# Kernel tuning notes

Measured on AMD Instinct MI355X. Metric: run time of the kernel, lower is better.

The kernel has to match this reference:

```python
import jax, jax.numpy as jnp
import numpy as np

N, E = 2048, 6144
DV_IN, DV_OUT = 128, 64
DE_IN, DE_OUT = 16, 16


def setup_inputs() -> dict:
    key = jax.random.key(0)
    ks = jax.random.split(key, 11)
    return {
        "H_v": jax.random.normal(ks[0], (N, DV_IN), jnp.float32),
        "H_e": jax.random.normal(ks[1], (E, DE_IN), jnp.float32),
        "adj_v": jax.random.uniform(ks[2], (N, N), jnp.float32),
        "adj_e": jax.random.uniform(ks[3], (E, E), jnp.float32),
        "T": jax.random.normal(ks[4], (N, E), jnp.float32),
        "W_v": jax.random.normal(ks[5], (DV_IN, DV_OUT), jnp.float32) * (1.0 / np.sqrt(DV_OUT)),
        "b_v": jax.random.normal(ks[6], (DV_OUT,), jnp.float32) * 0.01,
        "p_v": jax.random.normal(ks[7], (1, DE_IN), jnp.float32),
        "W_e": jax.random.normal(ks[8], (DE_IN, DE_OUT), jnp.float32) * (1.0 / np.sqrt(DE_OUT)),
        "b_e": jax.random.normal(ks[9], (DE_OUT,), jnp.float32) * 0.01,
        "p_e": jax.random.normal(ks[10], (1, DV_OUT), jnp.float32),
    }


def reference(H_v, H_e, adj_v, adj_e, T, W_v, b_v, p_v, W_e, b_e, p_e):
    n, e = T.shape
    # ---- node layer (AlternateConvolution, node_layer=True) ----
    d_e = (H_e @ p_v.T)[:, 0]                      # [E] per-edge diag values
    mult1 = (T * d_e[None, :]) @ T.T               # T @ diag(d_e) @ T^T -> [N,N]
    idx_n = jnp.arange(n)
    M1 = mult1.at[idx_n, idx_n].set(1.0)           # eye*1 + (1-eye)*multiplier
    adjusted_Av = M1 * adj_v
    Hv_out = adjusted_Av @ (H_v @ W_v) + b_v       # [N, DV_OUT]
    # ---- edge layer (AlternateConvolution, node_layer=False) ----
    d_v = (Hv_out @ p_e.T)[:, 0]                   # [N] per-node diag values
    mult2 = (T.T * d_v[None, :]) @ T               # T^T @ diag(d_v) @ T -> [E,E]
    idx_e = jnp.arange(e)
    M2 = mult2.at[idx_e, idx_e].set(1.0)
    adjusted_Ae = M2 * adj_e
    norm_Ae = adjusted_Ae / (adjusted_Ae.max(axis=0, keepdims=True) + 1e-10)
    He_out = norm_Ae @ (H_e @ W_e) + b_e           # [E, DE_OUT]
    return Hv_out, He_out
```

## Files before the change

### kernel.cpp

```cpp
#include <hip/hip_runtime.h>

typedef unsigned short u16;
typedef unsigned int u32;
typedef __bf16 bf16x8 __attribute__((ext_vector_type(8)));
typedef float f32x4 __attribute__((ext_vector_type(4)));

#define NN 2048
#define NE 6144
#define DVIN 128
#define DVOUT 64
#define DEIN 16
#define DEOUT 16

#define BM 128
#define BN 128
#define BK 64
#define MS 132

__device__ __forceinline__ u16 f2b(float f) {
  __bf16 b = (__bf16)f;
  return __builtin_bit_cast(u16, b);
}

__device__ __forceinline__ float b2f(u16 u) {
  return __uint_as_float(((u32)u) << 16);
}

__device__ __forceinline__ void async16(const void* g, void* l) {
  __builtin_amdgcn_global_load_lds(
      (const __attribute__((address_space(1))) void*)g,
      (__attribute__((address_space(3))) void*)l, 16, 0, 0);
}

__device__ __forceinline__ bf16x8 load8(const u16* p) {
  union { uint4 u; bf16x8 b; } w;
  w.u = *(const uint4*)p;
  return w.b;
}


__global__ __launch_bounds__(256) void k_de(const float* __restrict__ He,
                                            const float* __restrict__ pv,
                                            float* __restrict__ de) {
  int j = blockIdx.x * 256 + threadIdx.x;
  float s = 0.f;
#pragma unroll
  for (int k = 0; k < DEIN; k++) s += He[j * DEIN + k] * pv[k];
  de[j] = s;
}

__global__ __launch_bounds__(256) void k_tb(const float* __restrict__ T,
                                            const float* __restrict__ de,
                                            u16* __restrict__ Tb,
                                            u16* __restrict__ Tbs) {
  size_t idx = (size_t)blockIdx.x * 256 + threadIdx.x;
  size_t f = idx * 8;
  float4 v0 = *(const float4*)(T + f);
  float4 v1 = *(const float4*)(T + f + 4);
  int col = (int)(f % (size_t)NE);
  float4 d0 = *(const float4*)(de + col);
  float4 d1 = *(const float4*)(de + col + 4);
  float v[8] = {v0.x, v0.y, v0.z, v0.w, v1.x, v1.y, v1.z, v1.w};
  float d[8] = {d0.x, d0.y, d0.z, d0.w, d1.x, d1.y, d1.z, d1.w};
  union { u16 s[8]; uint4 u; } a, b;
#pragma unroll
  for (int j = 0; j < 8; j++) { a.s[j] = f2b(v[j]); b.s[j] = f2b(v[j] * d[j]); }
  *(uint4*)(Tb + f) = a.u;
  *(uint4*)(Tbs + f) = b.u;
}

__global__ __launch_bounds__(256) void k_x(const float* __restrict__ Hv,
                                           const float* __restrict__ Wv,
                                           u16* __restrict__ Xt) {
  int i = blockIdx.x * 256 + threadIdx.x;
  int d = blockIdx.y;
  float s = 0.f;
#pragma unroll 8
  for (int k = 0; k < DVIN; k++) s += Hv[i * DVIN + k] * Wv[k * DVOUT + d];
  Xt[(size_t)d * NN + i] = f2b(s);
}

__global__ __launch_bounds__(256) void k_dv(const float* __restrict__ HvOut,
                                            const float* __restrict__ pe,
                                            float* __restrict__ dv) {
  int i = blockIdx.x * 256 + threadIdx.x;
  float s = 0.f;
#pragma unroll
  for (int c = 0; c < DVOUT; c++) s += HvOut[i * DVOUT + c] * pe[c];
  dv[i] = s;
}

__global__ __launch_bounds__(256) void k_tt(const float* __restrict__ T,
                                            const float* __restrict__ dv,
                                            u16* __restrict__ Tt,
                                            u16* __restrict__ Tts) {
  __shared__ float tile[32][33];
  int tx = threadIdx.x, ty = threadIdx.y;
  int bx = blockIdx.x, by = blockIdx.y;
  int col = bx * 32 + tx;
#pragma unroll
  for (int r = 0; r < 4; r++) {
    int row = by * 32 + ty + r * 8;
    tile[ty + r * 8][tx] = T[(size_t)row * NE + col];
  }
  __syncthreads();
  int ocol = by * 32 + tx;
  float dvv = dv[ocol];
#pragma unroll
  for (int r = 0; r < 4; r++) {
    int orow = bx * 32 + ty + r * 8;
    float v = tile[tx][ty + r * 8];
    Tt[(size_t)orow * NN + ocol] = f2b(v);
    Tts[(size_t)orow * NN + ocol] = f2b(v * dvv);
  }
}

__global__ __launch_bounds__(256) void k_zt(const float* __restrict__ He,
                                            const float* __restrict__ We,
                                            const u32* __restrict__ colmax,
                                            u16* __restrict__ Ztb) {
  int b = blockIdx.x * 256 + threadIdx.x;
  float h[16];
  const float4* hp = (const float4*)(He + (size_t)b * DEIN);
#pragma unroll
  for (int q = 0; q < 4; q++) {
    float4 t = hp[q];
    h[q * 4 + 0] = t.x; h[q * 4 + 1] = t.y; h[q * 4 + 2] = t.z; h[q * 4 + 3] = t.w;
  }
  float inv = 1.0f / (__uint_as_float(colmax[b]) + 1e-10f);
#pragma unroll
  for (int d = 0; d < DEOUT; d++) {
    float s = 0.f;
#pragma unroll
    for (int k = 0; k < DEIN; k++) s += h[k] * We[k * DEOUT + d];
    Ztb[(size_t)d * NE + b] = f2b(s * inv);
  }
}

__device__ __forceinline__ void tile_loop(const u16* __restrict__ A,
                                          const u16* __restrict__ B,
                                          int bm0, int bn0, int K,
                                          int kbeg, int kend,
                                          u16* As, u16* Bs,
                                          f32x4 (&acc)[4][4]) {
  const int t = threadIdx.x;
  const int lane = t & 63;
  const int lr = lane & 15, kg = lane >> 4;
  const int wave = t >> 6;
  const int wm = (wave >> 1) * 64, wn = (wave & 1) * 64;

  const int arow = t >> 3;
  const int acolsw = (((t & 7) ^ (arow & 7)) * 8);
  const u16* Ag = A + (size_t)(bm0 + arow) * K + acolsw;
  const u16* Bg = B + (size_t)(bn0 + arow) * K + acolsw;
  u16* Al = &As[t * 8];
  u16* Bl = &Bs[t * 8];

  for (int k0 = kbeg; k0 < kend; k0 += BK) {
    __syncthreads();
#pragma unroll
    for (int r = 0; r < 4; r++) {
      async16(Ag + (size_t)(r * 32) * K + k0, Al + r * 32 * BK);
      async16(Bg + (size_t)(r * 32) * K + k0, Bl + r * 32 * BK);
    }
    __syncthreads();
#pragma unroll
    for (int kk = 0; kk < BK; kk += 32) {
      bf16x8 af[4], bf[4];
#pragma unroll
      for (int mi = 0; mi < 4; mi++) {
        int row = wm + mi * 16 + lr;
        int c = (kk >> 3) + kg;
        af[mi] = load8(&As[row * BK + ((c ^ (row & 7)) << 3)]);
      }
#pragma unroll
      for (int ni = 0; ni < 4; ni++) {
        int row = wn + ni * 16 + lr;
        int c = (kk >> 3) + kg;
        bf[ni] = load8(&Bs[row * BK + ((c ^ (row & 7)) << 3)]);
      }
#pragma unroll
      for (int mi = 0; mi < 4; mi++)
#pragma unroll
        for (int ni = 0; ni < 4; ni++)
          acc[mi][ni] = __builtin_amdgcn_mfma_f32_16x16x32_bf16(
              af[mi], bf[ni], acc[mi][ni], 0, 0, 0);
    }
  }
}

__global__ __launch_bounds__(256) void gemm_sym1(const u16* __restrict__ A,
                                                 const u16* __restrict__ B,
                                                 float* __restrict__ P) {
  const int bi = blockIdx.y, bj = blockIdx.x;
  if (bj < bi) return;
  __shared__ u16 As[BM * BK];
  __shared__ u16 Bs[BN * BK];
  const int bm0 = bi * BM, bn0 = bj * BN;
  const int K = NE, kc = NE / 4;
  f32x4 acc[4][4];
#pragma unroll
  for (int i = 0; i < 4; i++)
#pragma unroll
    for (int j = 0; j < 4; j++) acc[i][j] = (f32x4){0.f, 0.f, 0.f, 0.f};

  tile_loop(A, B, bm0, bn0, K, blockIdx.z * kc, (blockIdx.z + 1) * kc, As, Bs, acc);

  const int t = threadIdx.x, lane = t & 63, lr = lane & 15, kg = lane >> 4;
  const int wave = t >> 6, wm = (wave >> 1) * 64, wn = (wave & 1) * 64;
  float* Pz = P + (size_t)blockIdx.z * NN * NN;
#pragma unroll
  for (int ni = 0; ni < 4; ni++) {
    const int cj = bn0 + wn + ni * 16 + lr;
#pragma unroll
    for (int mi = 0; mi < 4; mi++)
#pragma unroll
      for (int r = 0; r < 4; r++) {
        const int ci = bm0 + wm + mi * 16 + kg * 4 + r;
        Pz[(size_t)ci * NN + cj] = acc[mi][ni][r];
      }
  }
}

__global__ __launch_bounds__(256) void k_comb(const float* __restrict__ P,
                                              const float* __restrict__ adj,
                                              u16* __restrict__ A1) {
  const int bi = blockIdx.y, bj = blockIdx.x;
  if (bj < bi) return;
  __shared__ float tile[128][129];
  const int bm0 = bi * 128, bn0 = bj * 128;
  const int t = threadIdx.x;
  const bool diagb = (bi == bj);
  const size_t NP = (size_t)NN * NN;
  for (int e = t; e < 128 * 32; e += 256) {
    int row = e >> 5, c4 = (e & 31) * 4;
    size_t off = (size_t)(bm0 + row) * NN + bn0 + c4;
    float4 s0 = *(const float4*)(P + off);
    float4 s1 = *(const float4*)(P + NP + off);
    float4 s2 = *(const float4*)(P + 2 * NP + off);
    float4 s3 = *(const float4*)(P + 3 * NP + off);
    float sv[4] = {s0.x + s1.x + s2.x + s3.x, s0.y + s1.y + s2.y + s3.y,
                   s0.z + s1.z + s2.z + s3.z, s0.w + s1.w + s2.w + s3.w};
    if (diagb) {
#pragma unroll
      for (int q = 0; q < 4; q++)
        if (c4 + q == row) sv[q] = 1.0f;
    }
    float4 av = *(const float4*)(adj + off);
    float avv[4] = {av.x, av.y, av.z, av.w};
    union { u16 h[4]; uint2 u; } o;
#pragma unroll
    for (int q = 0; q < 4; q++) {
      tile[row][c4 + q] = sv[q];
      o.h[q] = f2b(sv[q] * avv[q]);
    }
    *(uint2*)(A1 + off) = o.u;
  }
  if (!diagb) {
    __syncthreads();
    for (int e = t; e < 128 * 32; e += 256) {
      int row = e >> 5, c4 = (e & 31) * 4;
      size_t off = (size_t)(bn0 + row) * NN + bm0 + c4;
      float4 av = *(const float4*)(adj + off);
      float avv[4] = {av.x, av.y, av.z, av.w};
      union { u16 h[4]; uint2 u; } o;
#pragma unroll
      for (int q = 0; q < 4; q++) o.h[q] = f2b(tile[c4 + q][row] * avv[q]);
      *(uint2*)(A1 + off) = o.u;
    }
  }
}

__global__ __launch_bounds__(256) void gemm_sym2(const u16* __restrict__ A,
                                                 const u16* __restrict__ B,
                                                 const float* __restrict__ adj,
                                                 u16* __restrict__ C,
                                                 u32* __restrict__ colmax) {
  const int bi = blockIdx.y, bj = blockIdx.x;
  if (bj < bi) return;
  __shared__ union {
    struct { u16 As[BM * BK]; u16 Bs[BN * BK]; } s;
    u16 mir[128 * MS];
  } sh;
  __shared__ u32 cmaxN[128];
  __shared__ u32 cmaxM[128];
  const int bm0 = bi * BM, bn0 = bj * BN;
  const int t = threadIdx.x;
  const int N = NE, K = NN;
  const bool diagb = (bi == bj);
  if (t < 128) { cmaxN[t] = 0u; cmaxM[t] = 0u; }

  f32x4 acc[4][4];
#pragma unroll
  for (int i = 0; i < 4; i++)
#pragma unroll
    for (int j = 0; j < 4; j++) acc[i][j] = (f32x4){0.f, 0.f, 0.f, 0.f};

  tile_loop(A, B, bm0, bn0, K, 0, K, sh.s.As, sh.s.Bs, acc);

  const int lane = t & 63, lr = lane & 15, kg = lane >> 4;
  const int wave = t >> 6, wm = (wave >> 1) * 64, wn = (wave & 1) * 64;

  __syncthreads();

#pragma unroll
  for (int ni = 0; ni < 4; ni++) {
    const int cjl = wn + ni * 16 + lr;
    const int cj = bn0 + cjl;
    float cm = 0.f;
#pragma unroll
    for (int mi = 0; mi < 4; mi++) {
#pragma unroll
      for (int r = 0; r < 4; r++) {
        const int cil = wm + mi * 16 + kg * 4 + r;
        const int ci = bm0 + cil;
        float v = acc[mi][ni][r];
        if (ci == cj) v = 1.0f;
        float w = v * adj[(size_t)ci * N + cj];
        C[(size_t)ci * N + cj] = f2b(w);
        cm = fmaxf(cm, w);
        if (!diagb) sh.mir[cjl * MS + cil] = f2b(v);
      }
    }
    atomicMax(&cmaxN[cjl], __float_as_uint(cm));
  }

  if (!diagb) {
    __syncthreads();
    const int rb = t >> 4, cb = (t & 15) * 8;
    float rmax[8];
#pragma unroll
    for (int q = 0; q < 8; q++) rmax[q] = 0.f;
#pragma unroll
    for (int rr = 0; rr < 8; rr++) {
      const int row = rb + rr * 16;
      union { uint2 u; u16 s[4]; } w0, w1;
      w0.u = *(const uint2*)&sh.mir[row * MS + cb];
      w1.u = *(const uint2*)&sh.mir[row * MS + cb + 4];
      float f[8] = {b2f(w0.s[0]), b2f(w0.s[1]), b2f(w0.s[2]), b2f(w0.s[3]),
                    b2f(w1.s[0]), b2f(w1.s[1]), b2f(w1.s[2]), b2f(w1.s[3])};
      const float* ap = adj + (size_t)(bn0 + row) * N + bm0 + cb;
      float4 a0 = *(const float4*)ap;
      float4 a1 = *(const float4*)(ap + 4);
      float a[8] = {a0.x, a0.y, a0.z, a0.w, a1.x, a1.y, a1.z, a1.w};
      union { u16 s[8]; uint4 u; } o;
#pragma unroll
      for (int q = 0; q < 8; q++) {
        float w = f[q] * a[q];
        rmax[q] = fmaxf(rmax[q], w);
        o.s[q] = f2b(w);
      }
      *(uint4*)&C[(size_t)(bn0 + row) * N + bm0 + cb] = o.u;
    }
#pragma unroll
    for (int q = 0; q < 8; q++)
      atomicMax(&cmaxM[cb + q], __float_as_uint(rmax[q]));
  }

  __syncthreads();
  if (t < 128) {
    atomicMax(&colmax[bn0 + t], cmaxN[t]);
    if (!diagb) atomicMax(&colmax[bm0 + t], cmaxM[t]);
  }
}


__global__ __launch_bounds__(256) void k_hv(const u16* __restrict__ A1,
                                            const u16* __restrict__ Xt,
                                            const float* __restrict__ bv,
                                            float* __restrict__ out) {
  __shared__ float red[4 * 1024];
  const int t = threadIdx.x, wave = t >> 6, lane = t & 63;
  const int lr = lane & 15, kg = lane >> 4;
  const int m0 = blockIdx.x * 16;
  const int K = NN;
  f32x4 acc[4];
#pragma unroll
  for (int i = 0; i < 4; i++) acc[i] = (f32x4){0.f, 0.f, 0.f, 0.f};
  const int kbeg = wave * (K / 4), kend = kbeg + (K / 4);
  for (int k = kbeg; k < kend; k += 32) {
    bf16x8 af = load8(&A1[(size_t)(m0 + lr) * K + k + kg * 8]);
#pragma unroll
    for (int ni = 0; ni < 4; ni++) {
      bf16x8 bfr = load8(&Xt[(size_t)(ni * 16 + lr) * K + k + kg * 8]);
      acc[ni] = __builtin_amdgcn_mfma_f32_16x16x32_bf16(af, bfr, acc[ni], 0, 0, 0);
    }
  }
#pragma unroll
  for (int ni = 0; ni < 4; ni++)
#pragma unroll
    for (int r = 0; r < 4; r++)
      red[wave * 1024 + (kg * 4 + r) * 64 + ni * 16 + lr] = acc[ni][r];
  __syncthreads();
#pragma unroll
  for (int q = 0; q < 4; q++) {
    int e = t + 256 * q;
    int row = e >> 6, col = e & 63;
    float v = red[e] + red[1024 + e] + red[2048 + e] + red[3072 + e] + bv[col];
    out[(size_t)(m0 + row) * DVOUT + col] = v;
  }
}

__global__ __launch_bounds__(256) void k_he(const u16* __restrict__ adjE,
                                            const u16* __restrict__ Ztb,
                                            const float* __restrict__ be,
                                            float* __restrict__ out) {
  __shared__ float red[4 * 256];
  const int t = threadIdx.x, wave = t >> 6, lane = t & 63;
  const int lr = lane & 15, kg = lane >> 4;
  const int m0 = blockIdx.x * 16;
  const int K = NE;
  f32x4 acc = (f32x4){0.f, 0.f, 0.f, 0.f};
  const int kbeg = wave * (K / 4), kend = kbeg + (K / 4);
  for (int k = kbeg; k < kend; k += 32) {
    bf16x8 af = load8(&adjE[(size_t)(m0 + lr) * K + k + kg * 8]);
    bf16x8 bfr = load8(&Ztb[(size_t)lr * K + k + kg * 8]);
    acc = __builtin_amdgcn_mfma_f32_16x16x32_bf16(af, bfr, acc, 0, 0, 0);
  }
#pragma unroll
  for (int r = 0; r < 4; r++)
    red[wave * 256 + (kg * 4 + r) * 16 + lr] = acc[r];
  __syncthreads();
  {
    int row = t >> 4, col = t & 15;
    float v = red[t] + red[256 + t] + red[512 + t] + red[768 + t] + be[col];
    out[(size_t)(m0 + row) * DEOUT + col] = v;
  }
}

extern "C" void kernel_launch(void* const* d_in, const int* in_sizes, int n_in,
                              void* d_out, int out_size, void* d_ws, size_t ws_size,
                              hipStream_t stream) {
  const float* H_v = (const float*)d_in[0];
  const float* H_e = (const float*)d_in[1];
  const float* adj_v = (const float*)d_in[2];
  const float* adj_e = (const float*)d_in[3];
  const float* T = (const float*)d_in[4];
  const float* W_v = (const float*)d_in[5];
  const float* b_v = (const float*)d_in[6];
  const float* p_v = (const float*)d_in[7];
  const float* W_e = (const float*)d_in[8];
  const float* b_e = (const float*)d_in[9];
  const float* p_e = (const float*)d_in[10];
  float* outHv = (float*)d_out;
  float* outHe = (float*)d_out + NN * DVOUT;

  char* ws = (char*)d_ws;
  u16* Tb   = (u16*)(ws + 0);
  u16* Tbs  = (u16*)(ws + 25165824);
  u16* Tt   = (u16*)(ws + 50331648);
  u16* Tts  = (u16*)(ws + 75497472);
  u16* adjE = (u16*)(ws + 100663296);
  u16* A1   = (u16*)(ws + 176160768);
  u16* Xt   = (u16*)(ws + 184549376);
  u16* Ztb  = (u16*)(ws + 184811520);
  float* de = (float*)(ws + 185008128);
  float* dv = (float*)(ws + 185032704);
  u32* cmax = (u32*)(ws + 185040896);
  float* P = (float*)(ws + 50331648);

  k_de<<<NE / 256, 256, 0, stream>>>(H_e, p_v, de);
  k_tb<<<(NN * (size_t)NE) / 8 / 256, 256, 0, stream>>>(T, de, Tb, Tbs);
  k_x<<<dim3(NN / 256, DVOUT), 256, 0, stream>>>(H_v, W_v, Xt);
  gemm_sym1<<<dim3(NN / BN, NN / BM, 4), 256, 0, stream>>>(Tbs, Tb, P);
  k_comb<<<dim3(NN / 128, NN / 128), 256, 0, stream>>>(P, adj_v, A1);
  k_hv<<<NN / 16, 256, 0, stream>>>(A1, Xt, b_v, outHv);
  k_dv<<<NN / 256, 256, 0, stream>>>(outHv, p_e, dv);
  k_tt<<<dim3(NE / 32, NN / 32), dim3(32, 8), 0, stream>>>(T, dv, Tt, Tts);
  hipMemsetAsync(cmax, 0, NE * sizeof(u32), stream);
  gemm_sym2<<<dim3(NE / BN, NE / BM), 256, 0, stream>>>(Tts, Tt, adj_e, adjE, cmax);
  k_zt<<<NE / 256, 256, 0, stream>>>(H_e, W_e, cmax, Ztb);
  k_he<<<NE / 16, 256, 0, stream>>>(adjE, Ztb, b_e, outHe);
}
```

Before: 660.1 us.

## Launch only upper-triangle tiles, pack split-K partials, widen GEMV blocks

The symmetric GEMMs and the combine kernel now launch a 1D grid that covers only upper-triangle tiles, decoded with a sqrt-based triangular index, so lower-triangle blocks no longer launch just to exit. The split-K partials of gemm_sym1 are written as packed per-tile fragments with vector stores, and k_comb unpacks them through shared memory. This replaces strided scalar stores and shrinks the partial buffer. k_hv and k_he switch to 512 threads with 8-way K splits to add memory-level parallelism, at the cost of larger shared reduction buffers.

```diff
diff --git a/kernel.cpp b/kernel.cpp
--- a/kernel.cpp
+++ b/kernel.cpp
@@ -36,6 +36,15 @@
   union { uint4 u; bf16x8 b; } w;
   w.u = *(const uint4*)p;
   return w.b;
+}
+
+__device__ __forceinline__ void tri_decode(int L, int Nt, int& bi, int& bj) {
+  float Nf = (float)Nt + 0.5f;
+  int b = (int)(Nf - sqrtf(Nf * Nf - 2.0f * (float)L));
+  while (b * Nt - (b * (b - 1)) / 2 > L) b--;
+  while ((b + 1) * Nt - ((b + 1) * b) / 2 <= L) b++;
+  bi = b;
+  bj = b + (L - (b * Nt - (b * (b - 1)) / 2));
 }
 
 
@@ -192,72 +201,76 @@
 __global__ __launch_bounds__(256) void gemm_sym1(const u16* __restrict__ A,
                                                  const u16* __restrict__ B,
                                                  float* __restrict__ P) {
-  const int bi = blockIdx.y, bj = blockIdx.x;
-  if (bj < bi) return;
+  const int L = blockIdx.x;
+  const int z = L / 136, tri = L - z * 136;
+  int bi, bj;
+  tri_decode(tri, NN / BM, bi, bj);
   __shared__ u16 As[BM * BK];
   __shared__ u16 Bs[BN * BK];
   const int bm0 = bi * BM, bn0 = bj * BN;
-  const int K = NE, kc = NE / 4;
+  const int kc = NE / 4;
   f32x4 acc[4][4];
 #pragma unroll
   for (int i = 0; i < 4; i++)
 #pragma unroll
     for (int j = 0; j < 4; j++) acc[i][j] = (f32x4){0.f, 0.f, 0.f, 0.f};
 
-  tile_loop(A, B, bm0, bn0, K, blockIdx.z * kc, (blockIdx.z + 1) * kc, As, Bs, acc);
-
-  const int t = threadIdx.x, lane = t & 63, lr = lane & 15, kg = lane >> 4;
-  const int wave = t >> 6, wm = (wave >> 1) * 64, wn = (wave & 1) * 64;
-  float* Pz = P + (size_t)blockIdx.z * NN * NN;
-#pragma unroll
-  for (int ni = 0; ni < 4; ni++) {
-    const int cj = bn0 + wn + ni * 16 + lr;
-#pragma unroll
-    for (int mi = 0; mi < 4; mi++)
-#pragma unroll
-      for (int r = 0; r < 4; r++) {
-        const int ci = bm0 + wm + mi * 16 + kg * 4 + r;
-        Pz[(size_t)ci * NN + cj] = acc[mi][ni][r];
-      }
-  }
+  tile_loop(A, B, bm0, bn0, NE, z * kc, (z + 1) * kc, As, Bs, acc);
+
+  const int t = threadIdx.x;
+  f32x4* P4 = (f32x4*)(P + ((size_t)z * 136 + tri) * (BM * BN) + t * 64);
+#pragma unroll
+  for (int ni = 0; ni < 4; ni++)
+#pragma unroll
+    for (int mi = 0; mi < 4; mi++) P4[ni * 4 + mi] = acc[mi][ni];
 }
 
 __global__ __launch_bounds__(256) void k_comb(const float* __restrict__ P,
                                               const float* __restrict__ adj,
                                               u16* __restrict__ A1) {
-  const int bi = blockIdx.y, bj = blockIdx.x;
-  if (bj < bi) return;
+  const int tri = blockIdx.x;
+  int bi, bj;
+  tri_decode(tri, NN / BM, bi, bj);
   __shared__ float tile[128][129];
   const int bm0 = bi * 128, bn0 = bj * 128;
   const int t = threadIdx.x;
   const bool diagb = (bi == bj);
-  const size_t NP = (size_t)NN * NN;
+  const int lane = t & 63, lr = lane & 15, kg = lane >> 4;
+  const int wave = t >> 6, wm = (wave >> 1) * 64, wn = (wave & 1) * 64;
+
+  const f32x4* P4 = (const f32x4*)(P + (size_t)tri * (BM * BN) + t * 64);
+  const size_t SL = (size_t)136 * BM * BN / 4;
+#pragma unroll
+  for (int ni = 0; ni < 4; ni++) {
+#pragma unroll
+    for (int mi = 0; mi < 4; mi++) {
+      f32x4 s = P4[ni * 4 + mi];
+      f32x4 s1 = P4[SL + ni * 4 + mi];
+      f32x4 s2 = P4[2 * SL + ni * 4 + mi];
+      f32x4 s3 = P4[3 * SL + ni * 4 + mi];
+      s = s + s1 + s2 + s3;
+      const int cil = wm + mi * 16 + kg * 4;
+      const int cjl = wn + ni * 16 + lr;
+#pragma unroll
+      for (int r = 0; r < 4; r++) tile[cil + r][cjl] = s[r];
+    }
+  }
+  __syncthreads();
   for (int e = t; e < 128 * 32; e += 256) {
     int row = e >> 5, c4 = (e & 31) * 4;
     size_t off = (size_t)(bm0 + row) * NN + bn0 + c4;
-    float4 s0 = *(const float4*)(P + off);
-    float4 s1 = *(const float4*)(P + NP + off);
-    float4 s2 = *(const float4*)(P + 2 * NP + off);
-    float4 s3 = *(const float4*)(P + 3 * NP + off);
-    float sv[4] = {s0.x + s1.x + s2.x + s3.x, s0.y + s1.y + s2.y + s3.y,
-                   s0.z + s1.z + s2.z + s3.z, s0.w + s1.w + s2.w + s3.w};
-    if (diagb) {
-#pragma unroll
-      for (int q = 0; q < 4; q++)
-        if (c4 + q == row) sv[q] = 1.0f;
-    }
     float4 av = *(const float4*)(adj + off);
     float avv[4] = {av.x, av.y, av.z, av.w};
     union { u16 h[4]; uint2 u; } o;
 #pragma unroll
     for (int q = 0; q < 4; q++) {
-      tile[row][c4 + q] = sv[q];
-      o.h[q] = f2b(sv[q] * avv[q]);
+      float sv = tile[row][c4 + q];
+      if (diagb && (c4 + q == row)) sv = 1.0f;
+      o.h[q] = f2b(sv * avv[q]);
     }
     *(uint2*)(A1 + off) = o.u;
   }
   if (!diagb) {
-    __syncthreads();
     for (int e = t; e < 128 * 32; e += 256) {
       int row = e >> 5, c4 = (e & 31) * 4;
       size_t off = (size_t)(bn0 + row) * NN + bm0 + c4;
@@ -276,8 +289,8 @@
                                                  const float* __restrict__ adj,
                                                  u16* __restrict__ C,
                                                  u32* __restrict__ colmax) {
-  const int bi = blockIdx.y, bj = blockIdx.x;
-  if (bj < bi) return;
+  int bi, bj;
+  tri_decode(blockIdx.x, NE / BM, bi, bj);
   __shared__ union {
     struct { u16 As[BM * BK]; u16 Bs[BN * BK]; } s;
     u16 mir[128 * MS];
@@ -365,11 +378,11 @@
 }
 
 
-__global__ __launch_bounds__(256) void k_hv(const u16* __restrict__ A1,
+__global__ __launch_bounds__(512) void k_hv(const u16* __restrict__ A1,
                                             const u16* __restrict__ Xt,
                                             const float* __restrict__ bv,
                                             float* __restrict__ out) {
-  __shared__ float red[4 * 1024];
+  __shared__ float red[8 * 1024];
   const int t = threadIdx.x, wave = t >> 6, lane = t & 63;
   const int lr = lane & 15, kg = lane >> 4;
   const int m0 = blockIdx.x * 16;
@@ -377,7 +390,7 @@
   f32x4 acc[4];
 #pragma unroll
   for (int i = 0; i < 4; i++) acc[i] = (f32x4){0.f, 0.f, 0.f, 0.f};
-  const int kbeg = wave * (K / 4), kend = kbeg + (K / 4);
+  const int kbeg = wave * (K / 8), kend = kbeg + (K / 8);
   for (int k = kbeg; k < kend; k += 32) {
     bf16x8 af = load8(&A1[(size_t)(m0 + lr) * K + k + kg * 8]);
 #pragma unroll
@@ -393,25 +406,27 @@
       red[wave * 1024 + (kg * 4 + r) * 64 + ni * 16 + lr] = acc[ni][r];
   __syncthreads();
 #pragma unroll
-  for (int q = 0; q < 4; q++) {
-    int e = t + 256 * q;
+  for (int q = 0; q < 2; q++) {
+    int e = t + 512 * q;
     int row = e >> 6, col = e & 63;
-    float v = red[e] + red[1024 + e] + red[2048 + e] + red[3072 + e] + bv[col];
+    float v = bv[col];
+#pragma unroll
+    for (int w = 0; w < 8; w++) v += red[w * 1024 + e];
     out[(size_t)(m0 + row) * DVOUT + col] = v;
   }
 }
 
-__global__ __launch_bounds__(256) void k_he(const u16* __restrict__ adjE,
+__global__ __launch_bounds__(512) void k_he(const u16* __restrict__ adjE,
                                             const u16* __restrict__ Ztb,
                                             const float* __restrict__ be,
                                             float* __restrict__ out) {
-  __shared__ float red[4 * 256];
+  __shared__ float red[8 * 256];
   const int t = threadIdx.x, wave = t >> 6, lane = t & 63;
   const int lr = lane & 15, kg = lane >> 4;
   const int m0 = blockIdx.x * 16;
   const int K = NE;
   f32x4 acc = (f32x4){0.f, 0.f, 0.f, 0.f};
-  const int kbeg = wave * (K / 4), kend = kbeg + (K / 4);
+  const int kbeg = wave * (K / 8), kend = kbeg + (K / 8);
   for (int k = kbeg; k < kend; k += 32) {
     bf16x8 af = load8(&adjE[(size_t)(m0 + lr) * K + k + kg * 8]);
     bf16x8 bfr = load8(&Ztb[(size_t)lr * K + k + kg * 8]);
@@ -421,9 +436,11 @@
   for (int r = 0; r < 4; r++)
     red[wave * 256 + (kg * 4 + r) * 16 + lr] = acc[r];
   __syncthreads();
-  {
+  if (t < 256) {
     int row = t >> 4, col = t & 15;
-    float v = red[t] + red[256 + t] + red[512 + t] + red[768 + t] + be[col];
+    float v = be[col];
+#pragma unroll
+    for (int w = 0; w < 8; w++) v += red[w * 256 + t];
     out[(size_t)(m0 + row) * DEOUT + col] = v;
   }
 }
@@ -462,13 +479,14 @@
   k_de<<<NE / 256, 256, 0, stream>>>(H_e, p_v, de);
   k_tb<<<(NN * (size_t)NE) / 8 / 256, 256, 0, stream>>>(T, de, Tb, Tbs);
   k_x<<<dim3(NN / 256, DVOUT), 256, 0, stream>>>(H_v, W_v, Xt);
-  gemm_sym1<<<dim3(NN / BN, NN / BM, 4), 256, 0, stream>>>(Tbs, Tb, P);
-  k_comb<<<dim3(NN / 128, NN / 128), 256, 0, stream>>>(P, adj_v, A1);
-  k_hv<<<NN / 16, 256, 0, stream>>>(A1, Xt, b_v, outHv);
+  gemm_sym1<<<4 * 136, 256, 0, stream>>>(Tbs, Tb, P);
+  k_comb<<<136, 256, 0, stream>>>(P, adj_v, A1);
+  k_hv<<<NN / 16, 512, 0, stream>>>(A1, Xt, b_v, outHv);
   k_dv<<<NN / 256, 256, 0, stream>>>(outHv, p_e, dv);
   k_tt<<<dim3(NE / 32, NN / 32), dim3(32, 8), 0, stream>>>(T, dv, Tt, Tts);
   hipMemsetAsync(cmax, 0, NE * sizeof(u32), stream);
-  gemm_sym2<<<dim3(NE / BN, NE / BM), 256, 0, stream>>>(Tts, Tt, adj_e, adjE, cmax);
+  gemm_sym2<<<(NE / BM) * (NE / BM + 1) / 2, 256, 0, stream>>>(
+      Tts, Tt, adj_e, adjE, cmax);
   k_zt<<<NE / 256, 256, 0, stream>>>(H_e, W_e, cmax, Ztb);
-  k_he<<<NE / 16, 256, 0, stream>>>(adjE, Ztb, b_e, outHe);
-}
+  k_he<<<NE / 16, 512, 0, stream>>>(adjE, Ztb, b_e, outHe);
+}
```

New measurement: 619.1 us. 1.07x faster.
